# Kernel optimization log

Measured on AMD Instinct MI355X. Metric: run time of the kernel, lower is better.

## Reference

```python
import jax, jax.numpy as jnp
import numpy as np

N = 100000          # nodes
E = 1600000         # edges
NODE_DIM = 128
HID = 64
NUM_LAYERS = 3
G = 256             # graphs in batch
BN_EPS = 1e-5


def setup_inputs() -> dict:
    key = jax.random.key(0)
    ks = jax.random.split(key, 20)
    x = jax.random.normal(ks[0], (N, NODE_DIM), dtype=jnp.float32)
    edge_index = jax.random.randint(ks[1], (2, E), 0, N, dtype=jnp.int64)
    batch = jnp.sort(jax.random.randint(ks[2], (N,), 0, G, dtype=jnp.int64))
    s_in = 1.0 / np.sqrt(NODE_DIM)
    s_h = 1.0 / np.sqrt(HID)
    W_in = jax.random.uniform(ks[3], (NODE_DIM, HID), jnp.float32, -s_in, s_in)
    b_in = jax.random.uniform(ks[4], (HID,), jnp.float32, -s_in, s_in)
    conv_W = jax.random.uniform(ks[5], (NUM_LAYERS, HID, HID), jnp.float32, -s_h, s_h)
    conv_b = jax.random.uniform(ks[6], (NUM_LAYERS, HID), jnp.float32, -s_h, s_h)
    bn_gamma = jnp.ones((NUM_LAYERS, HID), jnp.float32)
    bn_beta = jnp.zeros((NUM_LAYERS, HID), jnp.float32)
    bn_mean = 0.1 * jax.random.normal(ks[7], (NUM_LAYERS, HID), jnp.float32)
    bn_var = jnp.ones((NUM_LAYERS, HID), jnp.float32) + 0.1 * jax.random.uniform(ks[8], (NUM_LAYERS, HID))
    W1 = jax.random.uniform(ks[9], (HID, HID), jnp.float32, -s_h, s_h)
    b1 = jax.random.uniform(ks[10], (HID,), jnp.float32, -s_h, s_h)
    W2 = jax.random.uniform(ks[11], (HID, HID // 2), jnp.float32, -s_h, s_h)
    b2 = jax.random.uniform(ks[12], (HID // 2,), jnp.float32, -s_h, s_h)
    s_h2 = 1.0 / np.sqrt(HID // 2)
    W3 = jax.random.uniform(ks[13], (HID // 2, 1), jnp.float32, -s_h2, s_h2)
    b3 = jax.random.uniform(ks[14], (1,), jnp.float32, -s_h2, s_h2)
    return dict(x=x, edge_index=edge_index, batch=batch, W_in=W_in, b_in=b_in,
                conv_W=conv_W, conv_b=conv_b, bn_gamma=bn_gamma, bn_beta=bn_beta,
                bn_mean=bn_mean, bn_var=bn_var, W1=W1, b1=b1, W2=W2, b2=b2, W3=W3, b3=b3)


def reference(x, edge_index, batch, W_in, b_in, conv_W, conv_b,
              bn_gamma, bn_beta, bn_mean, bn_var, W1, b1, W2, b2, W3, b3):
    n = x.shape[0]
    loop = jnp.arange(n, dtype=edge_index.dtype)
    src = jnp.concatenate([edge_index[0], loop])   # edges + self loops
    dst = jnp.concatenate([edge_index[1], loop])
    deg = jax.ops.segment_sum(jnp.ones_like(src, dtype=x.dtype), dst, num_segments=n)
    dinv = jax.lax.rsqrt(jnp.maximum(deg, 1.0))
    norm = (dinv[src] * dinv[dst])[:, None]        # [E+N, 1] sym-normalized edge weight

    h = x @ W_in + b_in                            # input projection [N, HID]
    for l in range(NUM_LAYERS):
        hw = h @ conv_W[l]                         # GCNConv: transform then aggregate
        agg = jax.ops.segment_sum(hw[src] * norm, dst, num_segments=n) + conv_b[l]
        # BatchNorm (eval: running stats) + ReLU; dropout is identity in eval
        hnorm = (agg - bn_mean[l]) * jax.lax.rsqrt(bn_var[l] + BN_EPS)
        h = jax.nn.relu(hnorm * bn_gamma[l] + bn_beta[l])

    # global mean pool over graphs
    sums = jax.ops.segment_sum(h, batch, num_segments=G)
    cnts = jax.ops.segment_sum(jnp.ones((n,), h.dtype), batch, num_segments=G)
    g = sums / jnp.maximum(cnts, 1.0)[:, None]     # [G, HID]

    g = jax.nn.relu(g @ W1 + b1)
    g = jax.nn.relu(g @ W2 + b2)
    out = g @ W3 + b3                              # [G, 1]
    return out.squeeze(-1)
```

## Files before the change

kernel.cpp:

```cpp
#include <hip/hip_runtime.h>
#include <hip/hip_bf16.h>

#define NN 100000
#define EE 1600000
#define NODE_DIM 128
#define HID 64
#define NGRAPH 256
#define BN_EPS 1e-5f

#define NB 196
#define BW 512
#define CH 4096
#define NCHUNK 391
#define MHIST (NB * NCHUNK)
#define MAXB 12288

typedef __attribute__((ext_vector_type(8))) short short8;
typedef __attribute__((ext_vector_type(4))) float f32x4;

static __device__ __forceinline__ unsigned short f2bf(float f) {
    unsigned u = __float_as_uint(f);
    unsigned r = (u + 0x7fffu + ((u >> 16) & 1u)) >> 16;
    return (unsigned short)r;
}
static __device__ __forceinline__ float bf2f(unsigned short u) {
    return __uint_as_float(((unsigned)u) << 16);
}

#define I_OFF   0
#define I_DEG   100032
#define I_HIST  200064
#define I_HS    276864
#define I_BS    353664
#define I_BO    353792
#define I_PAIR  353920
#define I_SRCS  3553920
#define I_DINV  5153920
#define I_WC    5253952
#define I_WFA   5262208
#define I_WF1   5266304
#define I_WF2   5268352
#define I_BUFA  5270400
#define I_BUFB  8470400
#define I_SUMS  11670400
#define I_SCSH  11686784
#define I_WS    11687168

__global__ __launch_bounds__(256) void hist_k(const int* __restrict__ dst,
                                              int* __restrict__ hist) {
    __shared__ int h[NB];
    for (int i = threadIdx.x; i < NB; i += 256) h[i] = 0;
    __syncthreads();
    int base = blockIdx.x * CH + threadIdx.x;
    #pragma unroll
    for (int j = 0; j < 16; ++j) {
        int e = base + j * 256;
        if (e < EE) {
            int d = __builtin_nontemporal_load(dst + e);
            atomicAdd(&h[d >> 9], 1);
        }
    }
    __syncthreads();
    for (int i = threadIdx.x; i < NB; i += 256)
        hist[i * NCHUNK + blockIdx.x] = h[i];
}

__global__ void scan1_k(const int* __restrict__ in, int* __restrict__ part,
                        int* __restrict__ bsums, int n) {
    __shared__ int wsum[4];
    __shared__ int woff[4];
    int t = threadIdx.x;
    int base = blockIdx.x * 1024 + t * 4;
    int v0 = 0, v1 = 0, v2 = 0, v3 = 0;
    if (base + 3 < n) {
        v0 = in[base]; v1 = in[base + 1]; v2 = in[base + 2]; v3 = in[base + 3];
    } else {
        if (base     < n) v0 = in[base];
        if (base + 1 < n) v1 = in[base + 1];
        if (base + 2 < n) v2 = in[base + 2];
    }
    int s = v0 + v1 + v2 + v3;
    int lane = t & 63, wid = t >> 6;
    int x = s;
    #pragma unroll
    for (int d = 1; d < 64; d <<= 1) {
        int y = __shfl_up(x, d, 64);
        if (lane >= d) x += y;
    }
    if (lane == 63) wsum[wid] = x;
    __syncthreads();
    if (t == 0) {
        int r = 0;
        for (int w = 0; w < 4; ++w) { woff[w] = r; r += wsum[w]; }
        bsums[blockIdx.x] = r;
    }
    __syncthreads();
    int ex = woff[wid] + (x - s);
    if (base     < n) part[base]     = ex;
    if (base + 1 < n) part[base + 1] = ex + v0;
    if (base + 2 < n) part[base + 2] = ex + v0 + v1;
    if (base + 3 < n) part[base + 3] = ex + v0 + v1 + v2;
}

__global__ void scan2_k(const int* __restrict__ bsums, int* __restrict__ boffs, int nb) {
    __shared__ int wsum[2];
    __shared__ int woff2[2];
    int t = threadIdx.x;
    int v = (t < nb) ? bsums[t] : 0;
    int lane = t & 63, wid = t >> 6;
    int x = v;
    #pragma unroll
    for (int d = 1; d < 64; d <<= 1) {
        int y = __shfl_up(x, d, 64);
        if (lane >= d) x += y;
    }
    if (lane == 63) wsum[wid] = x;
    __syncthreads();
    if (t == 0) { woff2[0] = 0; woff2[1] = wsum[0]; }
    __syncthreads();
    int ex = woff2[wid] + (x - v);
    if (t < nb) boffs[t] = ex;
}

__global__ void scan3g_k(int* __restrict__ arr, const int* __restrict__ boffs, int n) {
    int i = blockIdx.x * 256 + threadIdx.x;
    if (i < n) arr[i] += boffs[i >> 10];
}

__global__ __launch_bounds__(256) void sortB_k(const int* __restrict__ srcA,
                                               const int* __restrict__ dstA,
                                               const int* __restrict__ hs,
                                               int2* __restrict__ pair) {
    __shared__ int lcur[NB];
    for (int i = threadIdx.x; i < NB; i += 256)
        lcur[i] = hs[i * NCHUNK + blockIdx.x];
    __syncthreads();
    int base = blockIdx.x * CH + threadIdx.x;
    #pragma unroll
    for (int j = 0; j < 16; ++j) {
        int e = base + j * 256;
        if (e < EE) {
            int d = __builtin_nontemporal_load(dstA + e);
            int s = __builtin_nontemporal_load(srcA + e);
            int pos = atomicAdd(&lcur[d >> 9], 1);
            pair[pos] = make_int2(d, s);
        }
    }
}

__global__ __launch_bounds__(256) void fineC_k(const int2* __restrict__ pair,
                                               const int* __restrict__ hs,
                                               int* __restrict__ deg,
                                               int* __restrict__ off,
                                               int* __restrict__ csrc) {
    __shared__ int cnt[BW];
    __shared__ int loff[BW];
    __shared__ int wsum[4];
    __shared__ int woff[4];
    __shared__ int ssrc[MAXB];
    int b = blockIdx.x;
    int t = threadIdx.x;
    int base = hs[b * NCHUNK];
    int end  = (b == NB - 1) ? EE : hs[(b + 1) * NCHUNK];
    int m = end - base;

    for (int i = t; i < BW; i += 256) cnt[i] = 0;
    __syncthreads();
    for (int i = t; i < m; i += 256) {
        int2 p = pair[base + i];
        atomicAdd(&cnt[p.x & (BW - 1)], 1);
    }
    __syncthreads();

    int c0 = cnt[2 * t], c1 = cnt[2 * t + 1];
    int s = c0 + c1;
    int lane = t & 63, wid = t >> 6;
    int x = s;
    #pragma unroll
    for (int d = 1; d < 64; d <<= 1) {
        int y = __shfl_up(x, d, 64);
        if (lane >= d) x += y;
    }
    if (lane == 63) wsum[wid] = x;
    __syncthreads();
    if (t == 0) {
        int r = 0;
        for (int w = 0; w < 4; ++w) { woff[w] = r; r += wsum[w]; }
    }
    __syncthreads();
    int ex = woff[wid] + (x - s);
    loff[2 * t] = ex;
    loff[2 * t + 1] = ex + c0;
    __syncthreads();

    int node0 = b << 9;
    for (int i = t; i < BW; i += 256) {
        int node = node0 + i;
        if (node < NN) { deg[node] = cnt[i]; off[node] = base + loff[i]; }
        else if (node == NN) { off[NN] = EE; }
    }
    __syncthreads();

    for (int i = t; i < BW; i += 256) cnt[i] = loff[i];
    __syncthreads();
    for (int i = t; i < m; i += 256) {
        int2 p = pair[base + i];
        int pos = atomicAdd(&cnt[p.x & (BW - 1)], 1);
        if (pos < MAXB) ssrc[pos] = p.y;
        else            csrc[base + pos] = p.y;
    }
    __syncthreads();
    int mm = m < MAXB ? m : MAXB;
    for (int i = t; i < mm; i += 256) csrc[base + i] = ssrc[i];
}

__global__ void dinv_k(const int* __restrict__ cnt, float* __restrict__ dinv, int n) {
    int i = blockIdx.x * 256 + threadIdx.x;
    if (i < n) dinv[i] = rsqrtf((float)(cnt[i] + 1));
}

__global__ void wsrc_k(const int* __restrict__ csrc, const float* __restrict__ dinv,
                       float* __restrict__ ws) {
    int e = blockIdx.x * 256 + threadIdx.x;
    if (e < EE) ws[e] = dinv[csrc[e]];
}

__global__ void bnprep_k(const float* __restrict__ convb, const float* __restrict__ gamma,
                         const float* __restrict__ beta, const float* __restrict__ mean,
                         const float* __restrict__ var, float* __restrict__ scsh) {
    int t = blockIdx.x * 64 + threadIdx.x;
    int l = t >> 6, c = t & 63;
    float sc = gamma[l * 64 + c] * rsqrtf(var[l * 64 + c] + BN_EPS);
    float sh = (convb[l * 64 + c] - mean[l * 64 + c]) * sc + beta[l * 64 + c];
    scsh[l * 128 + c] = sc;
    scsh[l * 128 + 64 + c] = sh;
}

__global__ void wc_k(const float* __restrict__ Win, const float* __restrict__ bin,
                     const float* __restrict__ cw0, float* __restrict__ Wc) {
    int idx = blockIdx.x * 256 + threadIdx.x;
    if (idx < NODE_DIM * HID) {
        int k = idx >> 6, c = idx & 63;
        float a = 0.f;
        #pragma unroll 8
        for (int j = 0; j < HID; ++j) a += Win[k * HID + j] * cw0[j * HID + c];
        Wc[idx] = a;
    } else if (idx < NODE_DIM * HID + HID) {
        int c = idx - NODE_DIM * HID;
        float a = 0.f;
        #pragma unroll 8
        for (int j = 0; j < HID; ++j) a += bin[j] * cw0[j * HID + c];
        Wc[idx] = a;
    }
}

__global__ __launch_bounds__(256) void wfrag_k(const float* __restrict__ Wc,
                                               const float* __restrict__ convW,
                                               short* __restrict__ WfA,
                                               short* __restrict__ Wf1,
                                               short* __restrict__ Wf2) {
    int id = blockIdx.x * 256 + threadIdx.x;
    const float* W; short* out; int u;
    if (id < 1024)      { W = Wc;           out = WfA; u = id; }
    else if (id < 1536) { W = convW + 4096; out = Wf1; u = id - 1024; }
    else                { W = convW + 8192; out = Wf2; u = id - 1536; }
    int l = u & 63, t = (u >> 6) & 3, s = u >> 8;
    int k0 = s * 32 + ((l >> 4) & 3) * 8;
    int col = t * 16 + (l & 15);
    short8 v;
    #pragma unroll
    for (int j = 0; j < 8; ++j) v[j] = (short)f2bf(W[(k0 + j) * 64 + col]);
    *(short8*)(out + u * 8) = v;
}

template <int K, bool BIAS, bool A_BF16>
__global__ __launch_bounds__(256, 4) void gemm_k(const void* __restrict__ inv,
                                                 const short8* __restrict__ Wf,
                                                 const float* __restrict__ bias,
                                                 __hip_bfloat16* __restrict__ out) {
    constexpr int NS = K / 32;
    int l = threadIdx.x & 63;
    int w = threadIdx.x >> 6;
    int rows0 = blockIdx.x * 64 + w * 16;
    int arow = rows0 + (l & 15);
    bool rok = arow < NN;
    int kgrp = (l >> 4) & 3;

    short8 wf[NS][4];
    #pragma unroll
    for (int s = 0; s < NS; ++s)
        #pragma unroll
        for (int t = 0; t < 4; ++t)
            wf[s][t] = Wf[(s * 4 + t) * 64 + l];

    f32x4 acc[4];
    #pragma unroll
    for (int t = 0; t < 4; ++t) acc[t] = (f32x4){0.f, 0.f, 0.f, 0.f};

    #pragma unroll
    for (int s = 0; s < NS; ++s) {
        short8 af = {0, 0, 0, 0, 0, 0, 0, 0};
        if (A_BF16) {
            if (rok)
                af = *(const short8*)((const short*)inv + (long)arow * K + s * 32 + kgrp * 8);
        } else {
            if (rok) {
                const float* ap = (const float*)inv + (long)arow * K + s * 32 + kgrp * 8;
                float4 a0 = *(const float4*)ap;
                float4 a1 = *(const float4*)(ap + 4);
                af[0] = (short)f2bf(a0.x); af[1] = (short)f2bf(a0.y);
                af[2] = (short)f2bf(a0.z); af[3] = (short)f2bf(a0.w);
                af[4] = (short)f2bf(a1.x); af[5] = (short)f2bf(a1.y);
                af[6] = (short)f2bf(a1.z); af[7] = (short)f2bf(a1.w);
            }
        }
        #pragma unroll
        for (int t = 0; t < 4; ++t)
            acc[t] = __builtin_amdgcn_mfma_f32_16x16x32_bf16(af, wf[s][t], acc[t], 0, 0, 0);
    }

    int orow0 = rows0 + kgrp * 4;
    #pragma unroll
    for (int t = 0; t < 4; ++t) {
        int col = t * 16 + (l & 15);
        float b = BIAS ? bias[col] : 0.f;
        #pragma unroll
        for (int r = 0; r < 4; ++r) {
            int row = orow0 + r;
            if (row < NN)
                out[(long)row * HID + col] = __float2bfloat16(acc[t][r] + b);
        }
    }
}

__global__ __launch_bounds__(256) void aggregate_k(const unsigned short* __restrict__ hw,
                                                   const int* __restrict__ off,
                                                   const int* __restrict__ src,
                                                   const float* __restrict__ ws,
                                                   const float* __restrict__ dinv,
                                                   const float* __restrict__ scsh,
                                                   unsigned short* __restrict__ out) {
    int lane = threadIdx.x & 63;
    int i = __builtin_amdgcn_readfirstlane((int)blockIdx.x * 4 + (threadIdx.x >> 6));
    float di = dinv[i];
    int e0 = off[i], e1 = off[i + 1];

    float acc = bf2f(hw[(long)i * HID + lane]) * di * di;

    int nit = (e1 - e0 + 7) >> 3;
    for (int it = 0; it < nit; ++it) {
        int eb = e0 + it * 8;
        int sx[8]; float wx[8];
        #pragma unroll
        for (int j = 0; j < 8; ++j) {
            int ee = eb + j;
            bool ok = ee < e1;
            sx[j] = src[ok ? ee : e0];
            wx[j] = ok ? ws[ee] * di : 0.f;
        }
        float h[8];
        #pragma unroll
        for (int j = 0; j < 8; ++j)
            h[j] = bf2f(hw[(long)sx[j] * HID + lane]);
        #pragma unroll
        for (int j = 0; j < 8; ++j)
            acc += h[j] * wx[j];
    }

    float sc = scsh[lane];
    float sh = scsh[64 + lane];
    out[(long)i * HID + lane] = f2bf(fmaxf(acc * sc + sh, 0.f));
}

__global__ __launch_bounds__(256) void pool1_k(const __hip_bfloat16* __restrict__ h,
                                               const int* __restrict__ batch,
                                               float* __restrict__ sums) {
    int lane = threadIdx.x & 63;
    int wid = threadIdx.x >> 6;
    int chunk = blockIdx.x * 4 + wid;
    int i0 = chunk * 64;
    if (i0 >= NN) return;
    int i1 = i0 + 64;
    if (i1 > NN) i1 = NN;
    int g = batch[i0];
    float acc = 0.f;
    for (int i = i0; i < i1; ++i) {
        int bi = batch[i];
        if (bi != g) {
            atomicAdd(&sums[g * HID + lane], acc);
            acc = 0.f;
            g = bi;
        }
        acc += __bfloat162float(h[(long)i * HID + lane]);
    }
    atomicAdd(&sums[g * HID + lane], acc);
}

__device__ __forceinline__ int lower_bound_i(const int* __restrict__ a, int n, int key) {
    int lo = 0, hi = n;
    while (lo < hi) {
        int m = (lo + hi) >> 1;
        if (a[m] < key) lo = m + 1; else hi = m;
    }
    return lo;
}

__global__ __launch_bounds__(64) void mlp_k(const float* __restrict__ sums,
                                            const int* __restrict__ batch,
                                            const float* __restrict__ W1, const float* __restrict__ b1,
                                            const float* __restrict__ W2, const float* __restrict__ b2,
                                            const float* __restrict__ W3, const float* __restrict__ b3,
                                            float* __restrict__ out) {
    int g = blockIdx.x;
    int lane = threadIdx.x;
    int start = lower_bound_i(batch, NN, g);
    int end = lower_bound_i(batch, NN, g + 1);
    float cnt = (float)(end - start);
    float gv = sums[g * HID + lane] / fmaxf(cnt, 1.0f);

    __shared__ float gs[HID];
    __shared__ float h1s[HID];
    gs[lane] = gv;
    __syncthreads();

    float a1 = b1[lane];
    #pragma unroll 8
    for (int k = 0; k < HID; ++k) a1 += gs[k] * W1[k * HID + lane];
    a1 = fmaxf(a1, 0.f);
    h1s[lane] = a1;
    __syncthreads();

    float a2 = 0.f;
    if (lane < 32) {
        a2 = b2[lane];
        #pragma unroll 8
        for (int k = 0; k < HID; ++k) a2 += h1s[k] * W2[k * 32 + lane];
        a2 = fmaxf(a2, 0.f);
    }
    float p = (lane < 32) ? a2 * W3[lane] : 0.f;
    #pragma unroll
    for (int d = 32; d >= 1; d >>= 1) p += __shfl_down(p, d, 64);
    if (lane == 0) out[g] = p + b3[0];
}

extern "C" void kernel_launch(void* const* d_in, const int* in_sizes, int n_in,
                              void* d_out, int out_size, void* d_ws, size_t ws_size,
                              hipStream_t stream) {
    (void)in_sizes; (void)n_in; (void)out_size; (void)ws_size;

    const float* x      = (const float*)d_in[0];
    const int*   eidx   = (const int*)d_in[1];
    const int*   batch  = (const int*)d_in[2];
    const float* W_in   = (const float*)d_in[3];
    const float* b_in   = (const float*)d_in[4];
    const float* conv_W = (const float*)d_in[5];
    const float* conv_b = (const float*)d_in[6];
    const float* gamma  = (const float*)d_in[7];
    const float* beta   = (const float*)d_in[8];
    const float* mean   = (const float*)d_in[9];
    const float* var    = (const float*)d_in[10];
    const float* W1     = (const float*)d_in[11];
    const float* b1     = (const float*)d_in[12];
    const float* W2     = (const float*)d_in[13];
    const float* b2     = (const float*)d_in[14];
    const float* W3     = (const float*)d_in[15];
    const float* b3     = (const float*)d_in[16];
    float* outp = (float*)d_out;

    int*   wsi = (int*)d_ws;
    float* wsf = (float*)d_ws;

    int*   off    = wsi + I_OFF;
    int*   deg    = wsi + I_DEG;
    int*   hist   = wsi + I_HIST;
    int*   hs     = wsi + I_HS;
    int*   bsums  = wsi + I_BS;
    int*   boffs  = wsi + I_BO;
    int2*  pair   = (int2*)(wsi + I_PAIR);
    int*   csrc   = wsi + I_SRCS;
    float* dinv   = wsf + I_DINV;
    float* Wc     = wsf + I_WC;
    short* WfA    = (short*)(wsi + I_WFA);
    short* Wf1    = (short*)(wsi + I_WF1);
    short* Wf2    = (short*)(wsi + I_WF2);
    __hip_bfloat16* bufA = (__hip_bfloat16*)(wsf + I_BUFA);
    __hip_bfloat16* bufB = (__hip_bfloat16*)(wsf + I_BUFB);
    float* sums   = wsf + I_SUMS;
    float* scsh   = wsf + I_SCSH;
    float* ws     = wsf + I_WS;

    const int* esrc = eidx;
    const int* edst = eidx + EE;

    hipMemsetAsync(sums, 0, NGRAPH * HID * sizeof(float), stream);

    hist_k<<<NCHUNK, 256, 0, stream>>>(edst, hist);
    int nb1 = (MHIST + 1023) / 1024;
    scan1_k<<<nb1, 256, 0, stream>>>(hist, hs, bsums, MHIST);
    scan2_k<<<1, 128, 0, stream>>>(bsums, boffs, nb1);
    scan3g_k<<<(MHIST + 255) / 256, 256, 0, stream>>>(hs, boffs, MHIST);
    wc_k<<<(NODE_DIM * HID + HID + 255) / 256, 256, 0, stream>>>(W_in, b_in, conv_W, Wc);
    wfrag_k<<<8, 256, 0, stream>>>(Wc, conv_W, WfA, Wf1, Wf2);
    bnprep_k<<<3, 64, 0, stream>>>(conv_b, gamma, beta, mean, var, scsh);
    sortB_k<<<NCHUNK, 256, 0, stream>>>(esrc, edst, hs, pair);
    fineC_k<<<NB, 256, 0, stream>>>(pair, hs, deg, off, csrc);
    dinv_k<<<(NN + 255) / 256, 256, 0, stream>>>(deg, dinv, NN);
    wsrc_k<<<(EE + 255) / 256, 256, 0, stream>>>(csrc, dinv, ws);

    int ngemm = (NN + 63) / 64;
    gemm_k<NODE_DIM, true, false><<<ngemm, 256, 0, stream>>>(x, (const short8*)WfA,
                                                             Wc + NODE_DIM * HID, bufA);
    aggregate_k<<<NN / 4, 256, 0, stream>>>((const unsigned short*)bufA, off, csrc, ws, dinv,
                                            scsh + 0 * 128, (unsigned short*)bufB);
    gemm_k<HID, false, true><<<ngemm, 256, 0, stream>>>(bufB, (const short8*)Wf1, nullptr, bufA);
    aggregate_k<<<NN / 4, 256, 0, stream>>>((const unsigned short*)bufA, off, csrc, ws, dinv,
                                            scsh + 1 * 128, (unsigned short*)bufB);
    gemm_k<HID, false, true><<<ngemm, 256, 0, stream>>>(bufB, (const short8*)Wf2, nullptr, bufA);
    aggregate_k<<<NN / 4, 256, 0, stream>>>((const unsigned short*)bufA, off, csrc, ws, dinv,
                                            scsh + 2 * 128, (unsigned short*)bufB);

    pool1_k<<<(NN / 64 + 3) / 4, 256, 0, stream>>>(bufB, batch, sums);
    mlp_k<<<NGRAPH, 64, 0, stream>>>(sums, batch, W1, b1, W2, b2, W3, b3, outp);
}
```

Measured before the change: 455.7 us.

## Replace per-node aggregation with edge-balanced block aggregation into shared memory

Measured after the change: 419.0 us. -8.1%, faster.

```diff
diff --git a/kernel.cpp b/kernel.cpp
--- a/kernel.cpp
+++ b/kernel.cpp
@@ -14,6 +14,8 @@
 #define NCHUNK 391
 #define MHIST (NB * NCHUNK)
 #define MAXB 12288
+
+#define DR 64
 
 typedef __attribute__((ext_vector_type(8))) short short8;
 typedef __attribute__((ext_vector_type(4))) float f32x4;
@@ -45,6 +47,7 @@
 #define I_SUMS  11670400
 #define I_SCSH  11686784
 #define I_WS    11687168
+#define I_DST   13287168
 
 __global__ __launch_bounds__(256) void hist_k(const int* __restrict__ dst,
                                               int* __restrict__ hist) {
@@ -152,12 +155,14 @@
                                                const int* __restrict__ hs,
                                                int* __restrict__ deg,
                                                int* __restrict__ off,
-                                               int* __restrict__ csrc) {
+                                               int* __restrict__ csrc,
+                                               int* __restrict__ cdst) {
     __shared__ int cnt[BW];
     __shared__ int loff[BW];
     __shared__ int wsum[4];
     __shared__ int woff[4];
     __shared__ int ssrc[MAXB];
+    __shared__ int sdst[MAXB];
     int b = blockIdx.x;
     int t = threadIdx.x;
     int base = hs[b * NCHUNK];
@@ -206,12 +211,15 @@
     for (int i = t; i < m; i += 256) {
         int2 p = pair[base + i];
         int pos = atomicAdd(&cnt[p.x & (BW - 1)], 1);
-        if (pos < MAXB) ssrc[pos] = p.y;
-        else            csrc[base + pos] = p.y;
+        if (pos < MAXB) { ssrc[pos] = p.y; sdst[pos] = p.x; }
+        else { csrc[base + pos] = p.y; cdst[base + pos] = p.x; }
     }
     __syncthreads();
     int mm = m < MAXB ? m : MAXB;
-    for (int i = t; i < mm; i += 256) csrc[base + i] = ssrc[i];
+    for (int i = t; i < mm; i += 256) {
+        csrc[base + i] = ssrc[i];
+        cdst[base + i] = sdst[i];
+    }
 }
 
 __global__ void dinv_k(const int* __restrict__ cnt, float* __restrict__ dinv, int n) {
@@ -333,43 +341,74 @@
     }
 }
 
-__global__ __launch_bounds__(256) void aggregate_k(const unsigned short* __restrict__ hw,
-                                                   const int* __restrict__ off,
-                                                   const int* __restrict__ src,
-                                                   const float* __restrict__ ws,
-                                                   const float* __restrict__ dinv,
-                                                   const float* __restrict__ scsh,
-                                                   unsigned short* __restrict__ out) {
-    int lane = threadIdx.x & 63;
-    int i = __builtin_amdgcn_readfirstlane((int)blockIdx.x * 4 + (threadIdx.x >> 6));
-    float di = dinv[i];
-    int e0 = off[i], e1 = off[i + 1];
-
-    float acc = bf2f(hw[(long)i * HID + lane]) * di * di;
-
-    int nit = (e1 - e0 + 7) >> 3;
-    for (int it = 0; it < nit; ++it) {
-        int eb = e0 + it * 8;
-        int sx[8]; float wx[8];
+__global__ __launch_bounds__(256) void agg2_k(const unsigned short* __restrict__ hw,
+                                              const int* __restrict__ off,
+                                              const int* __restrict__ csrc,
+                                              const int* __restrict__ cdst,
+                                              const float* __restrict__ ws,
+                                              const float* __restrict__ dinv,
+                                              const float* __restrict__ scsh,
+                                              unsigned short* __restrict__ out) {
+    __shared__ float accs[DR * HID];
+    int t = threadIdx.x;
+    int lane = t & 63;
+    int wid = t >> 6;
+    int d0 = blockIdx.x * DR;
+    int dhi = d0 + DR; if (dhi > NN) dhi = NN;
+
+    #pragma unroll
+    for (int j = 0; j < DR * HID / 256; ++j) accs[t + j * 256] = 0.f;
+    __syncthreads();
+
+    int e0b = off[d0];
+    int e1b = off[dhi];
+    int m = e1b - e0b;
+    int mw = (m + 3) >> 2;
+    int wstart = e0b + wid * mw;
+    int wend = wstart + mw; if (wend > e1b) wend = e1b;
+
+    float acc = 0.f;
+    int cur_d = -1;
+    for (int eb = wstart; eb < wend; eb += 64) {
+        int ee = eb + lane;
+        bool ok = ee < wend;
+        int svec = ok ? csrc[ee] : 0;
+        int dvec = ok ? cdst[ee] : -1;
+        float wvec = ok ? ws[ee] : 0.f;
+        int wbits = __float_as_uint(wvec);
         #pragma unroll
-        for (int j = 0; j < 8; ++j) {
-            int ee = eb + j;
-            bool ok = ee < e1;
-            sx[j] = src[ok ? ee : e0];
-            wx[j] = ok ? ws[ee] * di : 0.f;
+        for (int jb = 0; jb < 64; jb += 16) {
+            unsigned short hv[16];
+            #pragma unroll
+            for (int j = 0; j < 16; ++j) {
+                int s = __builtin_amdgcn_readlane(svec, jb + j);
+                hv[j] = hw[(long)s * HID + lane];
+            }
+            #pragma unroll
+            for (int j = 0; j < 16; ++j) {
+                int d = __builtin_amdgcn_readlane(dvec, jb + j);
+                float w = __uint_as_float((unsigned)__builtin_amdgcn_readlane(wbits, jb + j));
+                if (d != cur_d) {
+                    if (cur_d >= 0) atomicAdd(&accs[(cur_d - d0) * HID + lane], acc);
+                    acc = 0.f;
+                    cur_d = d;
+                }
+                acc += w * bf2f(hv[j]);
+            }
         }
-        float h[8];
-        #pragma unroll
-        for (int j = 0; j < 8; ++j)
-            h[j] = bf2f(hw[(long)sx[j] * HID + lane]);
-        #pragma unroll
-        for (int j = 0; j < 8; ++j)
-            acc += h[j] * wx[j];
-    }
+    }
+    if (cur_d >= 0) atomicAdd(&accs[(cur_d - d0) * HID + lane], acc);
+    __syncthreads();
 
     float sc = scsh[lane];
     float sh = scsh[64 + lane];
-    out[(long)i * HID + lane] = f2bf(fmaxf(acc * sc + sh, 0.f));
+    for (int dd = wid; dd < DR; dd += 4) {
+        int d = d0 + dd;
+        if (d >= NN) break;
+        float dv = dinv[d];
+        float v = (accs[dd * HID + lane] + bf2f(hw[(long)d * HID + lane]) * dv) * dv;
+        out[(long)d * HID + lane] = f2bf(fmaxf(v * sc + sh, 0.f));
+    }
 }
 
 __global__ __launch_bounds__(256) void pool1_k(const __hip_bfloat16* __restrict__ h,
@@ -478,6 +517,7 @@
     int*   boffs  = wsi + I_BO;
     int2*  pair   = (int2*)(wsi + I_PAIR);
     int*   csrc   = wsi + I_SRCS;
+    int*   cdst   = wsi + I_DST;
     float* dinv   = wsf + I_DINV;
     float* Wc     = wsf + I_WC;
     short* WfA    = (short*)(wsi + I_WFA);
@@ -503,21 +543,22 @@
     wfrag_k<<<8, 256, 0, stream>>>(Wc, conv_W, WfA, Wf1, Wf2);
     bnprep_k<<<3, 64, 0, stream>>>(conv_b, gamma, beta, mean, var, scsh);
     sortB_k<<<NCHUNK, 256, 0, stream>>>(esrc, edst, hs, pair);
-    fineC_k<<<NB, 256, 0, stream>>>(pair, hs, deg, off, csrc);
+    fineC_k<<<NB, 256, 0, stream>>>(pair, hs, deg, off, csrc, cdst);
     dinv_k<<<(NN + 255) / 256, 256, 0, stream>>>(deg, dinv, NN);
     wsrc_k<<<(EE + 255) / 256, 256, 0, stream>>>(csrc, dinv, ws);
 
     int ngemm = (NN + 63) / 64;
+    int nagg  = (NN + DR - 1) / DR;
     gemm_k<NODE_DIM, true, false><<<ngemm, 256, 0, stream>>>(x, (const short8*)WfA,
                                                              Wc + NODE_DIM * HID, bufA);
-    aggregate_k<<<NN / 4, 256, 0, stream>>>((const unsigned short*)bufA, off, csrc, ws, dinv,
-                                            scsh + 0 * 128, (unsigned short*)bufB);
+    agg2_k<<<nagg, 256, 0, stream>>>((const unsigned short*)bufA, off, csrc, cdst, ws, dinv,
+                                     scsh + 0 * 128, (unsigned short*)bufB);
     gemm_k<HID, false, true><<<ngemm, 256, 0, stream>>>(bufB, (const short8*)Wf1, nullptr, bufA);
-    aggregate_k<<<NN / 4, 256, 0, stream>>>((const unsigned short*)bufA, off, csrc, ws, dinv,
-                                            scsh + 1 * 128, (unsigned short*)bufB);
+    agg2_k<<<nagg, 256, 0, stream>>>((const unsigned short*)bufA, off, csrc, cdst, ws, dinv,
+                                     scsh + 1 * 128, (unsigned short*)bufB);
     gemm_k<HID, false, true><<<ngemm, 256, 0, stream>>>(bufB, (const short8*)Wf2, nullptr, bufA);
-    aggregate_k<<<NN / 4, 256, 0, stream>>>((const unsigned short*)bufA, off, csrc, ws, dinv,
-                                            scsh + 2 * 128, (unsigned short*)bufB);
+    agg2_k<<<nagg, 256, 0, stream>>>((const unsigned short*)bufA, off, csrc, cdst, ws, dinv,
+                                     scsh + 2 * 128, (unsigned short*)bufB);
 
     pool1_k<<<(NN / 64 + 3) / 4, 256, 0, stream>>>(bufB, batch, sums);
     mlp_k<<<NGRAPH, 64, 0, stream>>>(sums, batch, W1, b1, W2, b2, W3, b3, outp);
```

## Aggregate over flat edge ranges per wave with explicit self-loops in CSR

Applied to the files above, without the earlier changes.

Result: faster. 411.8 us (-9.6%).

```diff
diff --git a/kernel.cpp b/kernel.cpp
--- a/kernel.cpp
+++ b/kernel.cpp
@@ -3,6 +3,7 @@
 
 #define NN 100000
 #define EE 1600000
+#define ETOT 1700000
 #define NODE_DIM 128
 #define HID 64
 #define NGRAPH 256
@@ -10,10 +11,12 @@
 
 #define NB 196
 #define BW 512
-#define CH 4096
-#define NCHUNK 391
+#define CH 16384
+#define NCHUNK 98
 #define MHIST (NB * NCHUNK)
 #define MAXB 12288
+
+#define GD 16
 
 typedef __attribute__((ext_vector_type(8))) short short8;
 typedef __attribute__((ext_vector_type(4))) float f32x4;
@@ -30,21 +33,22 @@
 #define I_OFF   0
 #define I_DEG   100032
 #define I_HIST  200064
-#define I_HS    276864
-#define I_BS    353664
-#define I_BO    353792
-#define I_PAIR  353920
-#define I_SRCS  3553920
-#define I_DINV  5153920
-#define I_WC    5253952
-#define I_WFA   5262208
-#define I_WF1   5266304
-#define I_WF2   5268352
-#define I_BUFA  5270400
-#define I_BUFB  8470400
-#define I_SUMS  11670400
-#define I_SCSH  11686784
-#define I_WS    11687168
+#define I_HS    219328
+#define I_BS    238592
+#define I_BO    238720
+#define I_PAIR  238848
+#define I_SRCS  3438848
+#define I_DST   5138944
+#define I_WS    6839040
+#define I_DINV  8539136
+#define I_WC    8639168
+#define I_WFA   8647424
+#define I_WF1   8651520
+#define I_WF2   8653568
+#define I_BUFA  8655616
+#define I_BUFB  11855616
+#define I_SUMS  15055616
+#define I_SCSH  15072000
 
 __global__ __launch_bounds__(256) void hist_k(const int* __restrict__ dst,
                                               int* __restrict__ hist) {
@@ -52,8 +56,7 @@
     for (int i = threadIdx.x; i < NB; i += 256) h[i] = 0;
     __syncthreads();
     int base = blockIdx.x * CH + threadIdx.x;
-    #pragma unroll
-    for (int j = 0; j < 16; ++j) {
+    for (int j = 0; j < CH / 256; ++j) {
         int e = base + j * 256;
         if (e < EE) {
             int d = __builtin_nontemporal_load(dst + e);
@@ -136,8 +139,7 @@
         lcur[i] = hs[i * NCHUNK + blockIdx.x];
     __syncthreads();
     int base = blockIdx.x * CH + threadIdx.x;
-    #pragma unroll
-    for (int j = 0; j < 16; ++j) {
+    for (int j = 0; j < CH / 256; ++j) {
         int e = base + j * 256;
         if (e < EE) {
             int d = __builtin_nontemporal_load(dstA + e);
@@ -152,27 +154,38 @@
                                                const int* __restrict__ hs,
                                                int* __restrict__ deg,
                                                int* __restrict__ off,
-                                               int* __restrict__ csrc) {
+                                               int* __restrict__ csrc,
+                                               int* __restrict__ cdst) {
     __shared__ int cnt[BW];
     __shared__ int loff[BW];
     __shared__ int wsum[4];
     __shared__ int woff[4];
     __shared__ int ssrc[MAXB];
+    __shared__ int sdst[MAXB];
     int b = blockIdx.x;
     int t = threadIdx.x;
-    int base = hs[b * NCHUNK];
-    int end  = (b == NB - 1) ? EE : hs[(b + 1) * NCHUNK];
-    int m = end - base;
+    int base_r = hs[b * NCHUNK];
+    int end_r  = (b == NB - 1) ? EE : hs[(b + 1) * NCHUNK];
+    int m = end_r - base_r;
+    int node0 = b << 9;
+    int base_out = base_r + b * BW;
 
     for (int i = t; i < BW; i += 256) cnt[i] = 0;
     __syncthreads();
     for (int i = t; i < m; i += 256) {
-        int2 p = pair[base + i];
+        int2 p = pair[base_r + i];
         atomicAdd(&cnt[p.x & (BW - 1)], 1);
     }
     __syncthreads();
 
-    int c0 = cnt[2 * t], c1 = cnt[2 * t + 1];
+    for (int i = t; i < BW; i += 256) {
+        int node = node0 + i;
+        if (node < NN) deg[node] = cnt[i];
+    }
+
+    int va = (node0 + 2 * t)     < NN ? 1 : 0;
+    int vb = (node0 + 2 * t + 1) < NN ? 1 : 0;
+    int c0 = cnt[2 * t] + va, c1 = cnt[2 * t + 1] + vb;
     int s = c0 + c1;
     int lane = t & 63, wid = t >> 6;
     int x = s;
@@ -193,25 +206,40 @@
     loff[2 * t + 1] = ex + c0;
     __syncthreads();
 
-    int node0 = b << 9;
     for (int i = t; i < BW; i += 256) {
         int node = node0 + i;
-        if (node < NN) { deg[node] = cnt[i]; off[node] = base + loff[i]; }
-        else if (node == NN) { off[NN] = EE; }
-    }
-    __syncthreads();
-
-    for (int i = t; i < BW; i += 256) cnt[i] = loff[i];
-    __syncthreads();
+        if (node < NN) off[node] = base_out + loff[i];
+        else if (node == NN) off[NN] = ETOT;
+    }
+
+    for (int i = t; i < BW; i += 256) {
+        int node = node0 + i;
+        int p = loff[i];
+        if (node < NN) {
+            if (p < MAXB) { ssrc[p] = node; sdst[p] = node; }
+            else { csrc[base_out + p] = node; cdst[base_out + p] = node; }
+            cnt[i] = p + 1;
+        } else {
+            cnt[i] = p;
+        }
+    }
+    __syncthreads();
+
     for (int i = t; i < m; i += 256) {
-        int2 p = pair[base + i];
+        int2 p = pair[base_r + i];
         int pos = atomicAdd(&cnt[p.x & (BW - 1)], 1);
-        if (pos < MAXB) ssrc[pos] = p.y;
-        else            csrc[base + pos] = p.y;
-    }
-    __syncthreads();
-    int mm = m < MAXB ? m : MAXB;
-    for (int i = t; i < mm; i += 256) csrc[base + i] = ssrc[i];
+        if (pos < MAXB) { ssrc[pos] = p.y; sdst[pos] = p.x; }
+        else { csrc[base_out + pos] = p.y; cdst[base_out + pos] = p.x; }
+    }
+    __syncthreads();
+
+    int nvalid = (b == NB - 1) ? (NN - node0) : BW;
+    int mo = m + nvalid;
+    int mm = mo < MAXB ? mo : MAXB;
+    for (int i = t; i < mm; i += 256) {
+        csrc[base_out + i] = ssrc[i];
+        cdst[base_out + i] = sdst[i];
+    }
 }
 
 __global__ void dinv_k(const int* __restrict__ cnt, float* __restrict__ dinv, int n) {
@@ -222,7 +250,7 @@
 __global__ void wsrc_k(const int* __restrict__ csrc, const float* __restrict__ dinv,
                        float* __restrict__ ws) {
     int e = blockIdx.x * 256 + threadIdx.x;
-    if (e < EE) ws[e] = dinv[csrc[e]];
+    if (e < ETOT) ws[e] = dinv[csrc[e]];
 }
 
 __global__ void bnprep_k(const float* __restrict__ convb, const float* __restrict__ gamma,
@@ -333,43 +361,70 @@
     }
 }
 
-__global__ __launch_bounds__(256) void aggregate_k(const unsigned short* __restrict__ hw,
-                                                   const int* __restrict__ off,
-                                                   const int* __restrict__ src,
-                                                   const float* __restrict__ ws,
-                                                   const float* __restrict__ dinv,
-                                                   const float* __restrict__ scsh,
-                                                   unsigned short* __restrict__ out) {
+__global__ __launch_bounds__(256) void agg3_k(const unsigned short* __restrict__ hw,
+                                              const int* __restrict__ off,
+                                              const int* __restrict__ csrc,
+                                              const int* __restrict__ cdst,
+                                              const float* __restrict__ ws,
+                                              const float* __restrict__ dinv,
+                                              const float* __restrict__ scsh,
+                                              unsigned short* __restrict__ out) {
     int lane = threadIdx.x & 63;
-    int i = __builtin_amdgcn_readfirstlane((int)blockIdx.x * 4 + (threadIdx.x >> 6));
-    float di = dinv[i];
-    int e0 = off[i], e1 = off[i + 1];
-
-    float acc = bf2f(hw[(long)i * HID + lane]) * di * di;
-
-    int nit = (e1 - e0 + 7) >> 3;
-    for (int it = 0; it < nit; ++it) {
-        int eb = e0 + it * 8;
-        int sx[8]; float wx[8];
-        #pragma unroll
-        for (int j = 0; j < 8; ++j) {
-            int ee = eb + j;
-            bool ok = ee < e1;
-            sx[j] = src[ok ? ee : e0];
-            wx[j] = ok ? ws[ee] * di : 0.f;
-        }
-        float h[8];
-        #pragma unroll
-        for (int j = 0; j < 8; ++j)
-            h[j] = bf2f(hw[(long)sx[j] * HID + lane]);
-        #pragma unroll
-        for (int j = 0; j < 8; ++j)
-            acc += h[j] * wx[j];
-    }
-
+    int wid = threadIdx.x >> 6;
+    int dw0 = blockIdx.x * 64 + wid * GD;
+    if (dw0 >= NN) return;
+    int dw1 = dw0 + GD; if (dw1 > NN) dw1 = NN;
+    int e0 = off[dw0], e1 = off[dw1];
     float sc = scsh[lane];
     float sh = scsh[64 + lane];
-    out[(long)i * HID + lane] = f2bf(fmaxf(acc * sc + sh, 0.f));
+    const char* hwb = (const char*)hw;
+    int laneOfs = lane * 2;
+
+    int cur_d = -1;
+    float acc = 0.f;
+    for (int eb = e0; eb < e1; eb += 64) {
+        int ee = eb + lane;
+        bool ok = ee < e1;
+        int ec = ok ? ee : (e1 - 1);
+        int svec = csrc[ec];
+        int dvec = ok ? cdst[ec] : NN;
+        float wv = ok ? ws[ec] : 0.f;
+        unsigned sofs = ((unsigned)svec) << 7;
+        unsigned wbits = __float_as_uint(wv);
+
+        int dprev = __shfl_up(dvec, 1, 64);
+        unsigned long long bmask = __ballot(dvec != dprev);
+        int d00 = __builtin_amdgcn_readfirstlane(dvec);
+        if (d00 != cur_d) bmask |= 1ull; else bmask &= ~1ull;
+
+        #pragma unroll
+        for (int h = 0; h < 2; ++h) {
+            unsigned short hv[32];
+            #pragma unroll
+            for (int j = 0; j < 32; ++j) {
+                unsigned so = (unsigned)__builtin_amdgcn_readlane((int)sofs, h * 32 + j);
+                hv[j] = *(const unsigned short*)(hwb + so + laneOfs);
+            }
+            #pragma unroll
+            for (int j = 0; j < 32; ++j) {
+                int jj = h * 32 + j;
+                if ((bmask >> jj) & 1ull) {
+                    if (cur_d >= 0) {
+                        float v = acc * dinv[cur_d];
+                        out[(long)cur_d * HID + lane] = f2bf(fmaxf(v * sc + sh, 0.f));
+                    }
+                    acc = 0.f;
+                    cur_d = __builtin_amdgcn_readlane(dvec, jj);
+                }
+                float w = __uint_as_float((unsigned)__builtin_amdgcn_readlane((int)wbits, jj));
+                acc += w * bf2f(hv[j]);
+            }
+        }
+    }
+    if (cur_d >= 0 && cur_d < NN) {
+        float v = acc * dinv[cur_d];
+        out[(long)cur_d * HID + lane] = f2bf(fmaxf(v * sc + sh, 0.f));
+    }
 }
 
 __global__ __launch_bounds__(256) void pool1_k(const __hip_bfloat16* __restrict__ h,
@@ -478,6 +533,8 @@
     int*   boffs  = wsi + I_BO;
     int2*  pair   = (int2*)(wsi + I_PAIR);
     int*   csrc   = wsi + I_SRCS;
+    int*   cdst   = wsi + I_DST;
+    float* ws     = wsf + I_WS;
     float* dinv   = wsf + I_DINV;
     float* Wc     = wsf + I_WC;
     short* WfA    = (short*)(wsi + I_WFA);
@@ -487,7 +544,6 @@
     __hip_bfloat16* bufB = (__hip_bfloat16*)(wsf + I_BUFB);
     float* sums   = wsf + I_SUMS;
     float* scsh   = wsf + I_SCSH;
-    float* ws     = wsf + I_WS;
 
     const int* esrc = eidx;
     const int* edst = eidx + EE;
@@ -503,21 +559,22 @@
     wfrag_k<<<8, 256, 0, stream>>>(Wc, conv_W, WfA, Wf1, Wf2);
     bnprep_k<<<3, 64, 0, stream>>>(conv_b, gamma, beta, mean, var, scsh);
     sortB_k<<<NCHUNK, 256, 0, stream>>>(esrc, edst, hs, pair);
-    fineC_k<<<NB, 256, 0, stream>>>(pair, hs, deg, off, csrc);
+    fineC_k<<<NB, 256, 0, stream>>>(pair, hs, deg, off, csrc, cdst);
     dinv_k<<<(NN + 255) / 256, 256, 0, stream>>>(deg, dinv, NN);
-    wsrc_k<<<(EE + 255) / 256, 256, 0, stream>>>(csrc, dinv, ws);
+    wsrc_k<<<(ETOT + 255) / 256, 256, 0, stream>>>(csrc, dinv, ws);
 
     int ngemm = (NN + 63) / 64;
+    int nagg  = (NN + 63) / 64;
     gemm_k<NODE_DIM, true, false><<<ngemm, 256, 0, stream>>>(x, (const short8*)WfA,
                                                              Wc + NODE_DIM * HID, bufA);
-    aggregate_k<<<NN / 4, 256, 0, stream>>>((const unsigned short*)bufA, off, csrc, ws, dinv,
-                                            scsh + 0 * 128, (unsigned short*)bufB);
+    agg3_k<<<nagg, 256, 0, stream>>>((const unsigned short*)bufA, off, csrc, cdst, ws, dinv,
+                                     scsh + 0 * 128, (unsigned short*)bufB);
     gemm_k<HID, false, true><<<ngemm, 256, 0, stream>>>(bufB, (const short8*)Wf1, nullptr, bufA);
-    aggregate_k<<<NN / 4, 256, 0, stream>>>((const unsigned short*)bufA, off, csrc, ws, dinv,
-                                            scsh + 1 * 128, (unsigned short*)bufB);
+    agg3_k<<<nagg, 256, 0, stream>>>((const unsigned short*)bufA, off, csrc, cdst, ws, dinv,
+                                     scsh + 1 * 128, (unsigned short*)bufB);
     gemm_k<HID, false, true><<<ngemm, 256, 0, stream>>>(bufB, (const short8*)Wf2, nullptr, bufA);
-    aggregate_k<<<NN / 4, 256, 0, stream>>>((const unsigned short*)bufA, off, csrc, ws, dinv,
-                                            scsh + 2 * 128, (unsigned short*)bufB);
+    agg3_k<<<nagg, 256, 0, stream>>>((const unsigned short*)bufA, off, csrc, cdst, ws, dinv,
+                                     scsh + 2 * 128, (unsigned short*)bufB);
 
     pool1_k<<<(NN / 64 + 3) / 4, 256, 0, stream>>>(bufB, batch, sums);
     mlp_k<<<NGRAPH, 64, 0, stream>>>(sums, batch, W1, b1, W2, b2, W3, b3, outp);
```
